# Kernel optimization log

Measured on AMD Instinct MI355X. Metric: run time of the kernel, lower is better.

## Reference

```python
import jax, jax.numpy as jnp
import numpy as np

D = 128
K = 8  # 2**(bits-1) centroids, bits=4 -> mse_bits=3
N = 131072
EPS = 1e-8


def setup_inputs() -> dict:
    key = jax.random.key(0)
    k_x, k_pi, k_c = jax.random.split(key, 3)
    x = jax.random.normal(k_x, (N, D), dtype=jnp.float32)
    # Random orthogonal rotation matrix (as produced from a seeded RNG in PolarQuant)
    Pi, _ = jnp.linalg.qr(jax.random.normal(k_pi, (D, D), dtype=jnp.float32))
    # Scalar codebook: K sorted centroids (nearest-centroid per coordinate)
    centroids = jnp.sort(jax.random.normal(k_c, (K,), dtype=jnp.float32))
    return {"x": x, "Pi": Pi, "centroids": centroids}


def reference(x, Pi, centroids):
    # --- quantize ---
    vec_norm = jnp.linalg.norm(x, axis=-1, keepdims=True)          # (N,1)
    x_normalized = x / (vec_norm + EPS)
    x_rotated = x_normalized @ Pi.T                                 # (N,D)
    # nearest-centroid search per coordinate against 1-D codebook
    d2 = jnp.square(x_rotated[..., None] - centroids)               # (N,D,K)
    mse_indices = jnp.argmin(d2, axis=-1)                           # (N,D) int
    x_mse_rotated = centroids[mse_indices]                          # (N,D)
    residual_rotated = x_rotated - x_mse_rotated
    residual_signs = jnp.where(residual_rotated >= 0, 1.0, -1.0).astype(x.dtype)
    residual_scale = jnp.mean(jnp.abs(residual_rotated), axis=-1)   # (N,)
    # --- dequantize with residual sign correction ---
    x_corrected_rotated = x_mse_rotated + residual_scale[:, None] * residual_signs
    x_corrected = x_corrected_rotated @ Pi                          # unrotate
    return x_corrected * vec_norm                                   # (N,D)
```

## Files before the change

### kernel.cpp

```cpp
#include <hip/hip_runtime.h>
#include <cstdint>

#define DIM 128
#define NCEN 8

typedef __attribute__((ext_vector_type(8))) short short8;
typedef __attribute__((ext_vector_type(4))) float f32x4;

constexpr int BLOCK = 512;
constexpr int WAVES = 8;
constexpr int RPG = 4;
constexpr int GROUPS = 4;
constexpr int ROWS_PER_BLOCK = WAVES * RPG * GROUPS;
constexpr int ROW_BYTES = 512;

__device__ __forceinline__ unsigned bf16rne(float f) {
    unsigned u = __float_as_uint(f);
    return (u + 0x7FFFu + ((u >> 16) & 1u)) >> 16;
}

__global__ __launch_bounds__(BLOCK, 4)
void pq_phase1(const float* __restrict__ x,
               const float* __restrict__ Pi,
               const float* __restrict__ cen,
               char* __restrict__ zout)
{
    __shared__ __align__(16) float lds_pi[DIM * DIM];
    __shared__ __align__(16) float xbuf[WAVES][RPG][DIM];

    const int tid  = threadIdx.x;
    const int wave = tid >> 6;
    const int lane = tid & 63;

    float cv[NCEN];
#pragma unroll
    for (int i = 0; i < NCEN; ++i) cv[i] = cen[i];

#pragma unroll
    for (int i = 0; i < 8; ++i) {
        int f = tid * 4 + i * (BLOCK * 4);
        int a = f >> 7;
        int b = f & 127;
        float4 v = *reinterpret_cast<const float4*>(Pi + f);
        *reinterpret_cast<float4*>(&lds_pi[a * 128 + (b ^ (a & 28))]) = v;
    }
    __syncthreads();

    const int d0 = 2 * lane;
    const int ca = d0 & 28;
    const float* prow0 = &lds_pi[(size_t)d0 * 128];
    const float* prow1 = prow0 + 128;

    const int row_block = blockIdx.x * ROWS_PER_BLOCK + wave * (RPG * GROUPS);

    const int lr   = lane >> 4;
    const int loff = (lane & 15) * 8;

    const float* xp0 = x + (size_t)(row_block + lr) * DIM + loff;
    float4 va = *reinterpret_cast<const float4*>(xp0);
    float4 vb = *reinterpret_cast<const float4*>(xp0 + 4);

    for (int g = 0; g < GROUPS; ++g) {
        const int r0 = row_block + g * RPG;

        *reinterpret_cast<float4*>(&xbuf[wave][lr][loff])     = va;
        *reinterpret_cast<float4*>(&xbuf[wave][lr][loff + 4]) = vb;

        float vn_l = 0.f, vne_l = 0.f;
        if (lane < 32) {
            const int row = lane >> 3;
            const int j   = lane & 7;
            const float* xr_ = &xbuf[wave][row][0];
            float v0 = xr_[j];
            float r  = __fmul_rn(v0, v0);
#pragma unroll
            for (int t = 1; t < 16; ++t) {
                float v = xr_[j + 8 * t];
                r = __fadd_rn(r, __fmul_rn(v, v));
            }
#pragma unroll
            for (int m = 1; m < 8; m <<= 1)
                r = __fadd_rn(r, __shfl_xor(r, m, 64));
            vn_l  = __fsqrt_rn(r);
            vne_l = __fadd_rn(vn_l, 1e-8f);
            if (j == 0)
                *reinterpret_cast<float*>(zout + (size_t)(r0 + row) * ROW_BYTES + 256) = vn_l;
        }
        const float vne = __shfl(vne_l, 8 * lr, 64);

        va.x = __fdiv_rn(va.x, vne); va.y = __fdiv_rn(va.y, vne);
        va.z = __fdiv_rn(va.z, vne); va.w = __fdiv_rn(va.w, vne);
        vb.x = __fdiv_rn(vb.x, vne); vb.y = __fdiv_rn(vb.y, vne);
        vb.z = __fdiv_rn(vb.z, vne); vb.w = __fdiv_rn(vb.w, vne);
        *reinterpret_cast<float4*>(&xbuf[wave][lr][loff])     = va;
        *reinterpret_cast<float4*>(&xbuf[wave][lr][loff + 4]) = vb;

        float4 va_n = va, vb_n = vb;
        if (g + 1 < GROUPS) {
            const float* xp = x + (size_t)(r0 + RPG + lr) * DIM + loff;
            va_n = *reinterpret_cast<const float4*>(xp);
            vb_n = *reinterpret_cast<const float4*>(xp + 4);
        }

        float acc[RPG][2];
#pragma unroll
        for (int r = 0; r < RPG; ++r) { acc[r][0] = 0.f; acc[r][1] = 0.f; }

#pragma unroll 8
        for (int k = 0; k < DIM; k += 4) {
            const int t0 = k ^ ca;
            float4 p0 = *reinterpret_cast<const float4*>(prow0 + t0);
            float4 p1 = *reinterpret_cast<const float4*>(prow1 + t0);
#pragma unroll
            for (int r = 0; r < RPG; ++r) {
                float4 xv = *reinterpret_cast<const float4*>(&xbuf[wave][r][k]);
                acc[r][0] = fmaf(xv.x, p0.x, acc[r][0]);
                acc[r][0] = fmaf(xv.y, p0.y, acc[r][0]);
                acc[r][0] = fmaf(xv.z, p0.z, acc[r][0]);
                acc[r][0] = fmaf(xv.w, p0.w, acc[r][0]);
                acc[r][1] = fmaf(xv.x, p1.x, acc[r][1]);
                acc[r][1] = fmaf(xv.y, p1.y, acc[r][1]);
                acc[r][1] = fmaf(xv.z, p1.z, acc[r][1]);
                acc[r][1] = fmaf(xv.w, p1.w, acc[r][1]);
            }
        }

        float qv[RPG][2], sg[RPG][2], asum[RPG];
#pragma unroll
        for (int r = 0; r < RPG; ++r) {
            asum[r] = 0.f;
#pragma unroll
            for (int j = 0; j < 2; ++j) {
                const float xr = acc[r][j];
                float dd   = __fsub_rn(xr, cv[0]);
                float best = __fmul_rn(dd, dd);
                float q    = cv[0];
#pragma unroll
                for (int i = 1; i < NCEN; ++i) {
                    float di = __fsub_rn(xr, cv[i]);
                    float d2 = __fmul_rn(di, di);
                    bool  c  = d2 < best;
                    best = c ? d2 : best;
                    q    = c ? cv[i] : q;
                }
                float res = __fsub_rn(xr, q);
                qv[r][j] = q;
                sg[r][j] = (res >= 0.f) ? 1.f : -1.f;
                asum[r] += fabsf(res);
            }
        }

#pragma unroll
        for (int r = 0; r < RPG; ++r) {
            float s = asum[r];
#pragma unroll
            for (int m = 1; m < 64; m <<= 1) s += __shfl_xor(s, m, 64);
            const float sc = s * (1.0f / 128.0f);
            float z0 = __fadd_rn(qv[r][0], sc * sg[r][0]);
            float z1 = __fadd_rn(qv[r][1], sc * sg[r][1]);
            unsigned pz = bf16rne(z0) | (bf16rne(z1) << 16);
            *reinterpret_cast<unsigned*>(zout + (size_t)(r0 + r) * ROW_BYTES + (size_t)d0 * 2) = pz;
        }

        va = va_n; vb = vb_n;
    }
}

constexpr int BBLOCK = 256;
constexpr int BROWS  = 256;

__global__ __launch_bounds__(BBLOCK, 8)
void pq_phase2(const float* __restrict__ Pi, char* __restrict__ zio)
{
    __shared__ __align__(16) unsigned short piT[DIM * DIM];

    const int tid  = threadIdx.x;
    const int wave = tid >> 6;
    const int lane = tid & 63;

#pragma unroll
    for (int s = 0; s < 4; ++s) {
        int sub = tid + s * BBLOCK;
        int a4 = (sub & 31) * 4;
        int b4 = (sub >> 5) * 4;
        float rv[4][4];
#pragma unroll
        for (int i = 0; i < 4; ++i)
            *reinterpret_cast<float4*>(rv[i]) =
                *reinterpret_cast<const float4*>(Pi + (size_t)(a4 + i) * DIM + b4);
#pragma unroll
        for (int j = 0; j < 4; ++j) {
            const int n   = b4 + j;
            const int ksw = a4 ^ ((n & 7) << 3);
            unsigned lo = bf16rne(rv[0][j]) | (bf16rne(rv[1][j]) << 16);
            unsigned hi = bf16rne(rv[2][j]) | (bf16rne(rv[3][j]) << 16);
            *reinterpret_cast<uint2*>(&piT[n * DIM + ksw]) = make_uint2(lo, hi);
        }
    }
    __syncthreads();

    const int rowbase0 = blockIdx.x * BROWS;

    for (int it = 0; it < BROWS / 64; ++it) {
        const int rowbase = rowbase0 + it * 64 + wave * 16;

        const char* zr = zio + (size_t)(rowbase + (lane & 15)) * ROW_BYTES + ((lane >> 4) * 16);
        short8 afr[4];
#pragma unroll
        for (int kf = 0; kf < 4; ++kf)
            afr[kf] = *reinterpret_cast<const short8*>(zr + kf * 64);

        float vnr[4];
#pragma unroll
        for (int q = 0; q < 4; ++q)
            vnr[q] = *reinterpret_cast<const float*>(
                zio + (size_t)(rowbase + (lane >> 4) * 4 + q) * ROW_BYTES + 256);

#pragma unroll
        for (int nt = 0; nt < 8; ++nt) {
            const int n = nt * 16 + (lane & 15);
            f32x4 acc = {0.f, 0.f, 0.f, 0.f};
#pragma unroll
            for (int kf = 0; kf < 4; ++kf) {
                const int k0  = kf * 32 + (lane >> 4) * 8;
                const int ksw = k0 ^ ((n & 7) << 3);
                short8 bfr = *reinterpret_cast<const short8*>(&piT[n * DIM + ksw]);
                acc = __builtin_amdgcn_mfma_f32_16x16x32_bf16(afr[kf], bfr, acc, 0, 0, 0);
            }
#pragma unroll
            for (int q = 0; q < 4; ++q) {
                float o = __fmul_rn(acc[q], vnr[q]);
                *reinterpret_cast<float*>(
                    zio + (size_t)(rowbase + (lane >> 4) * 4 + q) * ROW_BYTES
                        + (size_t)(nt * 16 + (lane & 15)) * 4) = o;
            }
        }
    }
}

extern "C" void kernel_launch(void* const* d_in, const int* in_sizes, int n_in,
                              void* d_out, int out_size, void* d_ws, size_t ws_size,
                              hipStream_t stream) {
    const float* x   = (const float*)d_in[0];
    const float* Pi  = (const float*)d_in[1];
    const float* cen = (const float*)d_in[2];
    char* outp       = (char*)d_out;

    const int n_rows = in_sizes[0] / DIM;

    hipLaunchKernelGGL(pq_phase1, dim3(n_rows / ROWS_PER_BLOCK), dim3(BLOCK), 0, stream,
                       x, Pi, cen, outp);
    hipLaunchKernelGGL(pq_phase2, dim3(n_rows / BROWS), dim3(BBLOCK), 0, stream,
                       Pi, outp);
}
```

Baseline: 122.2 us.

## Broadcast normalized x via readlane and interleave Pi rows in LDS for phase1

```diff
diff --git a/kernel.cpp b/kernel.cpp
--- a/kernel.cpp
+++ b/kernel.cpp
@@ -7,9 +7,9 @@
 typedef __attribute__((ext_vector_type(8))) short short8;
 typedef __attribute__((ext_vector_type(4))) float f32x4;
 
-constexpr int BLOCK = 512;
-constexpr int WAVES = 8;
-constexpr int RPG = 4;
+constexpr int BLOCK = 256;
+constexpr int WAVES = 4;
+constexpr int RPG = 8;
 constexpr int GROUPS = 4;
 constexpr int ROWS_PER_BLOCK = WAVES * RPG * GROUPS;
 constexpr int ROW_BYTES = 512;
@@ -18,151 +18,160 @@
     unsigned u = __float_as_uint(f);
     return (u + 0x7FFFu + ((u >> 16) & 1u)) >> 16;
 }
-
-__global__ __launch_bounds__(BLOCK, 4)
+__device__ __forceinline__ float rdlane(float v, int srclane) {
+    return __int_as_float(__builtin_amdgcn_readlane(__float_as_int(v), srclane));
+}
+
+__global__ __launch_bounds__(BLOCK, 2)
 void pq_phase1(const float* __restrict__ x,
                const float* __restrict__ Pi,
                const float* __restrict__ cen,
                char* __restrict__ zout)
 {
-    __shared__ __align__(16) float lds_pi[DIM * DIM];
+    __shared__ __align__(16) float p2[DIM * DIM];
     __shared__ __align__(16) float xbuf[WAVES][RPG][DIM];
 
     const int tid  = threadIdx.x;
     const int wave = tid >> 6;
     const int lane = tid & 63;
+    const int row  = lane >> 3;
+    const int jl   = lane & 7;
 
     float cv[NCEN];
 #pragma unroll
     for (int i = 0; i < NCEN; ++i) cv[i] = cen[i];
 
 #pragma unroll
-    for (int i = 0; i < 8; ++i) {
-        int f = tid * 4 + i * (BLOCK * 4);
-        int a = f >> 7;
-        int b = f & 127;
-        float4 v = *reinterpret_cast<const float4*>(Pi + f);
-        *reinterpret_cast<float4*>(&lds_pi[a * 128 + (b ^ (a & 28))]) = v;
+    for (int i = 0; i < 16; ++i) {
+        int chunk = i * BLOCK + tid;
+        int p = chunk >> 6, q = chunk & 63;
+        float2 r0 = *reinterpret_cast<const float2*>(Pi + (size_t)(2 * p) * DIM + 2 * q);
+        float2 r1 = *reinterpret_cast<const float2*>(Pi + (size_t)(2 * p + 1) * DIM + 2 * q);
+        int off = p * 256 + ((q * 4) ^ ((p & 7) << 2));
+        *reinterpret_cast<float4*>(p2 + off) = make_float4(r0.x, r1.x, r0.y, r1.y);
     }
     __syncthreads();
 
+    const int row_block = blockIdx.x * ROWS_PER_BLOCK + wave * (RPG * GROUPS);
     const int d0 = 2 * lane;
-    const int ca = d0 & 28;
-    const float* prow0 = &lds_pi[(size_t)d0 * 128];
-    const float* prow1 = prow0 + 128;
-
-    const int row_block = blockIdx.x * ROWS_PER_BLOCK + wave * (RPG * GROUPS);
-
-    const int lr   = lane >> 4;
-    const int loff = (lane & 15) * 8;
-
-    const float* xp0 = x + (size_t)(row_block + lr) * DIM + loff;
-    float4 va = *reinterpret_cast<const float4*>(xp0);
-    float4 vb = *reinterpret_cast<const float4*>(xp0 + 4);
+
+    float xr_[16], xn_[16];
+    {
+        const float* xp = x + (size_t)(row_block + row) * DIM + jl * 16;
+#pragma unroll
+        for (int c = 0; c < 4; ++c)
+            *reinterpret_cast<float4*>(&xr_[4 * c]) =
+                *reinterpret_cast<const float4*>(xp + 4 * c);
+    }
 
     for (int g = 0; g < GROUPS; ++g) {
-        const int r0 = row_block + g * RPG;
-
-        *reinterpret_cast<float4*>(&xbuf[wave][lr][loff])     = va;
-        *reinterpret_cast<float4*>(&xbuf[wave][lr][loff + 4]) = vb;
-
-        float vn_l = 0.f, vne_l = 0.f;
-        if (lane < 32) {
-            const int row = lane >> 3;
-            const int j   = lane & 7;
-            const float* xr_ = &xbuf[wave][row][0];
-            float v0 = xr_[j];
-            float r  = __fmul_rn(v0, v0);
-#pragma unroll
-            for (int t = 1; t < 16; ++t) {
-                float v = xr_[j + 8 * t];
-                r = __fadd_rn(r, __fmul_rn(v, v));
-            }
-#pragma unroll
-            for (int m = 1; m < 8; m <<= 1)
-                r = __fadd_rn(r, __shfl_xor(r, m, 64));
-            vn_l  = __fsqrt_rn(r);
-            vne_l = __fadd_rn(vn_l, 1e-8f);
-            if (j == 0)
-                *reinterpret_cast<float*>(zout + (size_t)(r0 + row) * ROW_BYTES + 256) = vn_l;
-        }
-        const float vne = __shfl(vne_l, 8 * lr, 64);
-
-        va.x = __fdiv_rn(va.x, vne); va.y = __fdiv_rn(va.y, vne);
-        va.z = __fdiv_rn(va.z, vne); va.w = __fdiv_rn(va.w, vne);
-        vb.x = __fdiv_rn(vb.x, vne); vb.y = __fdiv_rn(vb.y, vne);
-        vb.z = __fdiv_rn(vb.z, vne); vb.w = __fdiv_rn(vb.w, vne);
-        *reinterpret_cast<float4*>(&xbuf[wave][lr][loff])     = va;
-        *reinterpret_cast<float4*>(&xbuf[wave][lr][loff + 4]) = vb;
-
-        float4 va_n = va, vb_n = vb;
+        const int r0row = row_block + g * RPG;
+
+#pragma unroll
+        for (int c = 0; c < 4; ++c)
+            *reinterpret_cast<float4*>(&xbuf[wave][row][jl * 16 + 4 * c]) =
+                *reinterpret_cast<const float4*>(&xr_[4 * c]);
+
+        const float* xrow = &xbuf[wave][row][0];
+        float v0  = xrow[jl];
+        float racc = __fmul_rn(v0, v0);
+#pragma unroll
+        for (int t = 1; t < 16; ++t) {
+            float v = xrow[jl + 8 * t];
+            racc = __fadd_rn(racc, __fmul_rn(v, v));
+        }
+        racc = __fadd_rn(racc, __shfl_xor(racc, 1, 64));
+        racc = __fadd_rn(racc, __shfl_xor(racc, 2, 64));
+        racc = __fadd_rn(racc, __shfl_xor(racc, 4, 64));
+        float vn  = __fsqrt_rn(racc);
+        float vne = __fadd_rn(vn, 1e-8f);
+        if (jl == 0)
+            *reinterpret_cast<float*>(zout + (size_t)(r0row + row) * ROW_BYTES + 256) = vn;
+
+#pragma unroll
+        for (int c = 0; c < 16; ++c) xr_[c] = __fdiv_rn(xr_[c], vne);
+
         if (g + 1 < GROUPS) {
-            const float* xp = x + (size_t)(r0 + RPG + lr) * DIM + loff;
-            va_n = *reinterpret_cast<const float4*>(xp);
-            vb_n = *reinterpret_cast<const float4*>(xp + 4);
-        }
-
-        float acc[RPG][2];
-#pragma unroll
-        for (int r = 0; r < RPG; ++r) { acc[r][0] = 0.f; acc[r][1] = 0.f; }
-
-#pragma unroll 8
-        for (int k = 0; k < DIM; k += 4) {
-            const int t0 = k ^ ca;
-            float4 p0 = *reinterpret_cast<const float4*>(prow0 + t0);
-            float4 p1 = *reinterpret_cast<const float4*>(prow1 + t0);
-#pragma unroll
-            for (int r = 0; r < RPG; ++r) {
-                float4 xv = *reinterpret_cast<const float4*>(&xbuf[wave][r][k]);
-                acc[r][0] = fmaf(xv.x, p0.x, acc[r][0]);
-                acc[r][0] = fmaf(xv.y, p0.y, acc[r][0]);
-                acc[r][0] = fmaf(xv.z, p0.z, acc[r][0]);
-                acc[r][0] = fmaf(xv.w, p0.w, acc[r][0]);
-                acc[r][1] = fmaf(xv.x, p1.x, acc[r][1]);
-                acc[r][1] = fmaf(xv.y, p1.y, acc[r][1]);
-                acc[r][1] = fmaf(xv.z, p1.z, acc[r][1]);
-                acc[r][1] = fmaf(xv.w, p1.w, acc[r][1]);
-            }
-        }
-
-        float qv[RPG][2], sg[RPG][2], asum[RPG];
+            const float* xp = x + (size_t)(r0row + RPG + row) * DIM + jl * 16;
+#pragma unroll
+            for (int c = 0; c < 4; ++c)
+                *reinterpret_cast<float4*>(&xn_[4 * c]) =
+                    *reinterpret_cast<const float4*>(xp + 4 * c);
+        }
+
+        float2 acc[RPG];
+#pragma unroll
+        for (int r = 0; r < RPG; ++r) acc[r] = make_float2(0.f, 0.f);
+
+        const float* prow = p2 + lane * 256;
+        const int    swz  = (lane & 7) << 2;
+        for (int kb = 0; kb < 8; ++kb) {
+            float4 pv[8];
+#pragma unroll
+            for (int qq = 0; qq < 8; ++qq)
+                pv[qq] = *reinterpret_cast<const float4*>(prow + ((((kb * 8 + qq) * 4)) ^ swz));
+#pragma unroll
+            for (int kc = 0; kc < 16; ++kc) {
+                const float plo = (kc & 1) ? pv[kc >> 1].z : pv[kc >> 1].x;
+                const float phi = (kc & 1) ? pv[kc >> 1].w : pv[kc >> 1].y;
+#pragma unroll
+                for (int r = 0; r < RPG; ++r) {
+                    float sx = rdlane(xr_[kc], r * 8 + kb);
+                    acc[r].x = fmaf(sx, plo, acc[r].x);
+                    acc[r].y = fmaf(sx, phi, acc[r].y);
+                }
+            }
+        }
+
 #pragma unroll
         for (int r = 0; r < RPG; ++r) {
-            asum[r] = 0.f;
-#pragma unroll
-            for (int j = 0; j < 2; ++j) {
-                const float xr = acc[r][j];
-                float dd   = __fsub_rn(xr, cv[0]);
+            float q0, q1, s0, s1, as;
+            {
+                const float xrv = acc[r].x;
+                float dd   = __fsub_rn(xrv, cv[0]);
                 float best = __fmul_rn(dd, dd);
-                float q    = cv[0];
+                q0 = cv[0];
 #pragma unroll
                 for (int i = 1; i < NCEN; ++i) {
-                    float di = __fsub_rn(xr, cv[i]);
+                    float di = __fsub_rn(xrv, cv[i]);
                     float d2 = __fmul_rn(di, di);
                     bool  c  = d2 < best;
                     best = c ? d2 : best;
-                    q    = c ? cv[i] : q;
+                    q0   = c ? cv[i] : q0;
                 }
-                float res = __fsub_rn(xr, q);
-                qv[r][j] = q;
-                sg[r][j] = (res >= 0.f) ? 1.f : -1.f;
-                asum[r] += fabsf(res);
-            }
-        }
-
-#pragma unroll
-        for (int r = 0; r < RPG; ++r) {
-            float s = asum[r];
-#pragma unroll
-            for (int m = 1; m < 64; m <<= 1) s += __shfl_xor(s, m, 64);
-            const float sc = s * (1.0f / 128.0f);
-            float z0 = __fadd_rn(qv[r][0], sc * sg[r][0]);
-            float z1 = __fadd_rn(qv[r][1], sc * sg[r][1]);
+                float res = __fsub_rn(xrv, q0);
+                s0 = (res >= 0.f) ? 1.f : -1.f;
+                as = fabsf(res);
+            }
+            {
+                const float xrv = acc[r].y;
+                float dd   = __fsub_rn(xrv, cv[0]);
+                float best = __fmul_rn(dd, dd);
+                q1 = cv[0];
+#pragma unroll
+                for (int i = 1; i < NCEN; ++i) {
+                    float di = __fsub_rn(xrv, cv[i]);
+                    float d2 = __fmul_rn(di, di);
+                    bool  c  = d2 < best;
+                    best = c ? d2 : best;
+                    q1   = c ? cv[i] : q1;
+                }
+                float res = __fsub_rn(xrv, q1);
+                s1 = (res >= 0.f) ? 1.f : -1.f;
+                as += fabsf(res);
+            }
+#pragma unroll
+            for (int m = 1; m < 64; m <<= 1) as += __shfl_xor(as, m, 64);
+            const float sc = as * (1.0f / 128.0f);
+            float z0 = __fadd_rn(q0, sc * s0);
+            float z1 = __fadd_rn(q1, sc * s1);
             unsigned pz = bf16rne(z0) | (bf16rne(z1) << 16);
-            *reinterpret_cast<unsigned*>(zout + (size_t)(r0 + r) * ROW_BYTES + (size_t)d0 * 2) = pz;
-        }
-
-        va = va_n; vb = vb_n;
+            *reinterpret_cast<unsigned*>(
+                zout + (size_t)(r0row + r) * ROW_BYTES + (size_t)d0 * 2) = pz;
+        }
+
+#pragma unroll
+        for (int c = 0; c < 16; ++c) xr_[c] = xn_[c];
     }
 }
 
```

After: 159.9 us. 30.9% more time.
